# Kernel tuning notes

Measured on AMD Instinct MI355X. Metric: run time of the kernel, lower is better.

The kernel has to match this reference:

```python
import jax, jax.numpy as jnp
import numpy as np

B, T, U = 4, 256, 64
D_ENC = D_PRED = 512
JOINT = 1024
VOCAB = 1024


def setup_inputs() -> dict:
    key = jax.random.key(0)
    ks = jax.random.split(key, 8)
    s = lambda d: 1.0 / np.sqrt(d)
    return {
        "enc": jax.random.normal(ks[0], (B, T, D_ENC), jnp.float32),
        "pred": jax.random.normal(ks[1], (B, U, D_PRED), jnp.float32),
        "W_enc": jax.random.normal(ks[2], (D_ENC, JOINT), jnp.float32) * s(D_ENC),
        "b_enc": jnp.zeros((JOINT,), jnp.float32),
        "W_pred": jax.random.normal(ks[3], (D_PRED, JOINT), jnp.float32) * s(D_PRED),
        "b_pred": jnp.zeros((JOINT,), jnp.float32),
        "W_out": jax.random.normal(ks[4], (JOINT, VOCAB), jnp.float32) * s(JOINT),
        "b_out": jnp.zeros((VOCAB,), jnp.float32),
    }


def reference(enc, pred, W_enc, b_enc, W_pred, b_pred, W_out, b_out):
    # Dense projections to joint_dim
    enc_out = jnp.einsum("btd,dj->btj", enc, W_enc) + b_enc      # [B,T,J]
    pred_out = jnp.einsum("bud,dj->buj", pred, W_pred) + b_pred  # [B,U,J]
    # Broadcast add over (T,U), tanh, then vocab projection
    joint = jnp.tanh(enc_out[:, :, None, :] + pred_out[:, None, :, :])  # [B,T,U,J]
    logits = jnp.einsum("btuj,jv->btuv", joint, W_out) + b_out           # [B,T,U,V]
    return logits
```

## Files before the change

kernel.cpp:

```cpp
#include <hip/hip_runtime.h>
#include <hip/hip_bf16.h>


typedef __bf16 bf16x8 __attribute__((ext_vector_type(8)));
typedef float f32x4 __attribute__((ext_vector_type(4)));
typedef unsigned int u32x4 __attribute__((ext_vector_type(4)));
using bf16_t = __hip_bfloat16;

#define B_ 4
#define T_ 256
#define U_ 64
#define DE 512
#define JD 1024
#define VV 1024

__device__ __forceinline__ void gl2lds16(const void* g, void* l) {
  __builtin_amdgcn_global_load_lds(
      (__attribute__((address_space(1))) void*)(g),
      (__attribute__((address_space(3))) void*)(l), 16, 0, 0);
}

__device__ __forceinline__ float fast_tanh(float x) {
  float xx = fminf(fmaxf(x, -30.f), 30.f);
  float e = __expf(2.f * xx);
  return 1.f - 2.f * __builtin_amdgcn_rcpf(e + 1.f);
}

__device__ __forceinline__ void transpose_body(const float* __restrict__ src,
                                               bf16_t* __restrict__ dst,
                                               int K, int N, int bx, int by, int tid,
                                               float (*tile)[33]) {
  const int nt = bx * 32, kt = by * 32;
  const int tx = tid & 31, ty = tid >> 5;
#pragma unroll
  for (int i = 0; i < 4; ++i)
    tile[ty + i * 8][tx] = src[(size_t)(kt + ty + i * 8) * N + nt + tx];
  __syncthreads();
#pragma unroll
  for (int i = 0; i < 4; ++i)
    dst[(size_t)(nt + ty + i * 8) * K + kt + tx] = __float2bfloat16(tile[tx][ty + i * 8]);
}

__global__ __launch_bounds__(256) void prep_k(
    const float* __restrict__ enc, const float* __restrict__ pred,
    bf16_t* __restrict__ encb, bf16_t* __restrict__ predb,
    const float* __restrict__ W_enc, bf16_t* __restrict__ WtE,
    const float* __restrict__ W_pred, bf16_t* __restrict__ WtP,
    const float* __restrict__ W_out, bf16_t* __restrict__ WtO) {
  __shared__ float tile[32][33];
  const int bid = blockIdx.x, tid = threadIdx.x;
  if (bid < 640) {
    size_t i = ((size_t)bid * 256 + tid) * 4;
    const float* src;
    bf16_t* dst;
    if (i < (size_t)B_ * T_ * DE) { src = enc; dst = encb; }
    else { i -= (size_t)B_ * T_ * DE; src = pred; dst = predb; }
    f32x4 v = *(const f32x4*)(src + i);
    bf16_t o[4];
#pragma unroll
    for (int z = 0; z < 4; ++z) o[z] = __float2bfloat16(v[z]);
    *(unsigned long long*)(dst + i) = *(unsigned long long*)o;
  } else if (bid < 1152) {
    const int lb = bid - 640;
    transpose_body(W_enc, WtE, DE, JD, lb & 31, lb >> 5, tid, tile);
  } else if (bid < 1664) {
    const int lb = bid - 1152;
    transpose_body(W_pred, WtP, DE, JD, lb & 31, lb >> 5, tid, tile);
  } else {
    const int lb = bid - 1664;
    transpose_body(W_out, WtO, JD, VV, lb & 31, lb >> 5, tid, tile);
  }
}

__device__ __forceinline__ void proj_body(const bf16_t* __restrict__ A,
                                          const bf16_t* __restrict__ Bt,
                                          const float* __restrict__ bias,
                                          float* __restrict__ C,
                                          int m0, int n0, int N, int K) {
  __shared__ bf16_t sA[128 * 32];
  __shared__ bf16_t sB[128 * 32];
  const int tid = threadIdx.x;
  const int wave = tid >> 6, lane = tid & 63;
  const int wm = wave >> 1, wn = wave & 1;

  f32x4 acc[4][4] = {};

  for (int k0 = 0; k0 < K; k0 += 32) {
    __syncthreads();
#pragma unroll
    for (int r = 0; r < 2; ++r) {
      const int base = (wave + 4 * r) * 1024;
      const int row  = (base >> 6) + (lane >> 2);
      const int kel  = (lane & 3) * 8;
      gl2lds16(A  + (size_t)(m0 + row) * K + k0 + kel, (char*)sA + base);
      gl2lds16(Bt + (size_t)(n0 + row) * K + k0 + kel, (char*)sB + base);
    }
    __syncthreads();
    bf16x8 af[4], bfr[4];
    const int kq = (lane >> 4) * 8;
#pragma unroll
    for (int i = 0; i < 4; ++i) {
      af[i]  = *(const bf16x8*)(const void*)(sA + (wm * 64 + i * 16 + (lane & 15)) * 32 + kq);
      bfr[i] = *(const bf16x8*)(const void*)(sB + (wn * 64 + i * 16 + (lane & 15)) * 32 + kq);
    }
#pragma unroll
    for (int i = 0; i < 4; ++i)
#pragma unroll
      for (int j = 0; j < 4; ++j)
        acc[i][j] = __builtin_amdgcn_mfma_f32_16x16x32_bf16(af[i], bfr[j], acc[i][j], 0, 0, 0);
  }

  float bv[4];
#pragma unroll
  for (int j = 0; j < 4; ++j) bv[j] = bias[n0 + wn * 64 + j * 16 + (lane & 15)];
#pragma unroll
  for (int i = 0; i < 4; ++i) {
    const int row = m0 + wm * 64 + i * 16 + ((lane >> 4) << 2);
#pragma unroll
    for (int j = 0; j < 4; ++j) {
      const int col = n0 + wn * 64 + j * 16 + (lane & 15);
#pragma unroll
      for (int rr = 0; rr < 4; ++rr)
        C[(size_t)(row + rr) * N + col] = acc[i][j][rr] + bv[j];
    }
  }
}

__global__ __launch_bounds__(256) void proj2_k(
    const bf16_t* __restrict__ encb, const bf16_t* __restrict__ predb,
    const bf16_t* __restrict__ WtE, const bf16_t* __restrict__ WtP,
    const float* __restrict__ b_enc, const float* __restrict__ b_pred,
    float* __restrict__ enc_o, float* __restrict__ pred_o) {
  int bid = blockIdx.x;
  if (bid < 64) {
    proj_body(encb, WtE, b_enc, enc_o, (bid >> 3) * 128, (bid & 7) * 128, JD, DE);
  } else {
    bid -= 64;
    proj_body(predb, WtP, b_pred, pred_o, (bid >> 3) * 128, (bid & 7) * 128, JD, DE);
  }
}


__device__ __forceinline__ void stage_btile(const bf16_t* __restrict__ Bt,
                                            int n0, int k0, char* bb, int wave, int lane) {
  const int rw = lane >> 2;
  const int cl = lane & 3;
#pragma unroll
  for (int g = 0; g < 2; ++g) {
    const int r  = g * 128 + wave * 16 + rw;
    const int cg = cl ^ ((r >> 1) & 3);
    gl2lds16(Bt + (size_t)(n0 + r) * JD + k0 + cg * 8, bb + (g * 128 + wave * 16) * 64);
  }
}

__device__ __forceinline__ void load_ep(const float* __restrict__ enc_o,
                                        const float* __restrict__ pred_o,
                                        int m0, int r, int h, int k0,
                                        f32x4 e[4], f32x4 p[4]) {
  const int m = m0 + r;
  const int enc_row  = m >> 6;
  const int pred_row = ((m >> 14) << 6) | (m & 63);
  const float* pe = enc_o  + (size_t)enc_row  * JD + k0 + h * 16;
  const float* pp = pred_o + (size_t)pred_row * JD + k0 + h * 16;
#pragma unroll
  for (int q = 0; q < 4; ++q) {
    e[q] = *(const f32x4*)(pe + q * 4);
    p[q] = *(const f32x4*)(pp + q * 4);
  }
}

__device__ __forceinline__ void tanh_write_A(const f32x4 e[4], const f32x4 p[4],
                                             char* ab, int r, int h) {
  bf16_t vals[16];
#pragma unroll
  for (int q = 0; q < 4; ++q)
#pragma unroll
    for (int z = 0; z < 4; ++z)
      vals[q * 4 + z] = __float2bfloat16(fast_tanh(e[q][z] + p[q][z]));
  const int key = (r >> 1) & 3;
  *(u32x4*)(void*)(ab + r * 64 + ((2 * h)     ^ key) * 16) = ((const u32x4*)(const void*)vals)[0];
  *(u32x4*)(void*)(ab + r * 64 + ((2 * h + 1) ^ key) * 16) = ((const u32x4*)(const void*)vals)[1];
}

__global__ __launch_bounds__(512, 2) void vocab_fused_k(
    const float* __restrict__ enc_o,
    const float* __restrict__ pred_o,
    const bf16_t* __restrict__ Bt,
    const float* __restrict__ bias,
    float* __restrict__ C) {
  __shared__ char smem[65536];
  const int tid  = threadIdx.x;
  const int wave = tid >> 6, lane = tid & 63;
  const int wm = wave >> 2, wn = wave & 3;

  const int cpx = gridDim.x >> 3;
  const int b   = blockIdx.x;
  const int lb  = (b & 7) * cpx + (b >> 3);
  const int n0  = (lb & 3) * 256;
  const int m0  = (lb >> 2) * 256;

  const int ar = tid >> 1;
  const int ah = tid & 1;

  f32x4 acc[8][4] = {};
  const int NT = JD / 32;

  {
    f32x4 e[4], p[4];
    load_ep(enc_o, pred_o, m0, ar, ah, 0, e, p);
    tanh_write_A(e, p, smem, ar, ah);
    load_ep(enc_o, pred_o, m0, ar, ah, 32, e, p);
    tanh_write_A(e, p, smem + 16384, ar, ah);
  }
  stage_btile(Bt, n0, 0,  smem + 32768, wave, lane);
  stage_btile(Bt, n0, 32, smem + 49152, wave, lane);
  asm volatile("s_waitcnt vmcnt(2) lgkmcnt(0)" ::: "memory");
  __builtin_amdgcn_s_barrier();
  __builtin_amdgcn_sched_barrier(0);

  f32x4 e2[4], p2[4];
  load_ep(enc_o, pred_o, m0, ar, ah, 2 * 32, e2, p2);
  __builtin_amdgcn_sched_barrier(0);

  for (int t = 0; t < NT; ++t) {
    const char* ab = smem + (t & 1) * 16384;
    const char* bb = smem + 32768 + (t & 1) * 16384;
    const int kq = lane >> 4;

    bf16x8 bfr[4];
#pragma unroll
    for (int j = 0; j < 4; ++j) {
      const int rb = wn * 64 + j * 16 + (lane & 15);
      const int cb = kq ^ ((rb >> 1) & 3);
      bfr[j] = *(const bf16x8*)(const void*)(bb + rb * 64 + cb * 16);
    }
#pragma unroll
    for (int mh = 0; mh < 2; ++mh) {
      bf16x8 af[4];
#pragma unroll
      for (int i = 0; i < 4; ++i) {
        const int ra = wm * 128 + mh * 64 + i * 16 + (lane & 15);
        const int ca = kq ^ ((ra >> 1) & 3);
        af[i] = *(const bf16x8*)(const void*)(ab + ra * 64 + ca * 16);
      }
      __builtin_amdgcn_s_setprio(1);
#pragma unroll
      for (int i = 0; i < 4; ++i)
#pragma unroll
        for (int j = 0; j < 4; ++j)
          acc[mh * 4 + i][j] =
              __builtin_amdgcn_mfma_f32_16x16x32_bf16(af[i], bfr[j], acc[mh * 4 + i][j], 0, 0, 0);
      __builtin_amdgcn_s_setprio(0);
    }

    if (t + 1 < NT) {
      __builtin_amdgcn_sched_barrier(0);
      __builtin_amdgcn_s_barrier();
      if (t + 2 < NT) {
        stage_btile(Bt, n0, (t + 2) * 32, (char*)smem + 32768 + (t & 1) * 16384, wave, lane);
        tanh_write_A(e2, p2, (char*)smem + (t & 1) * 16384, ar, ah);
        asm volatile("s_waitcnt vmcnt(2) lgkmcnt(0)" ::: "memory");
      } else {
        asm volatile("s_waitcnt vmcnt(0) lgkmcnt(0)" ::: "memory");
      }
      __builtin_amdgcn_s_barrier();
      __builtin_amdgcn_sched_barrier(0);
      if (t + 3 < NT) {
        load_ep(enc_o, pred_o, m0, ar, ah, (t + 3) * 32, e2, p2);
        __builtin_amdgcn_sched_barrier(0);
      }
    }
  }

  float bv[4];
#pragma unroll
  for (int j = 0; j < 4; ++j) bv[j] = bias[n0 + wn * 64 + j * 16 + (lane & 15)];
#pragma unroll
  for (int i = 0; i < 8; ++i) {
    const int row = m0 + wm * 128 + i * 16 + ((lane >> 4) << 2);
#pragma unroll
    for (int j = 0; j < 4; ++j) {
      const int col = n0 + wn * 64 + j * 16 + (lane & 15);
#pragma unroll
      for (int rr = 0; rr < 4; ++rr)
        C[(size_t)(row + rr) * VV + col] = acc[i][j][rr] + bv[j];
    }
  }
}

extern "C" void kernel_launch(void* const* d_in, const int* in_sizes, int n_in,
                              void* d_out, int out_size, void* d_ws, size_t ws_size,
                              hipStream_t stream) {
  const float* enc    = (const float*)d_in[0];
  const float* pred   = (const float*)d_in[1];
  const float* W_enc  = (const float*)d_in[2];
  const float* b_enc  = (const float*)d_in[3];
  const float* W_pred = (const float*)d_in[4];
  const float* b_pred = (const float*)d_in[5];
  const float* W_out  = (const float*)d_in[6];
  const float* b_out  = (const float*)d_in[7];
  float* out = (float*)d_out;

  char* ws = (char*)d_ws;
  bf16_t* encb   = (bf16_t*)(ws + 0x000000);
  bf16_t* predb  = (bf16_t*)(ws + 0x100000);
  bf16_t* WtE    = (bf16_t*)(ws + 0x140000);
  bf16_t* WtP    = (bf16_t*)(ws + 0x240000);
  bf16_t* WtO    = (bf16_t*)(ws + 0x340000);
  float*  enc_o  = (float*) (ws + 0x540000);
  float*  pred_o = (float*) (ws + 0x940000);

  prep_k<<<2688, 256, 0, stream>>>(enc, pred, encb, predb, W_enc, WtE, W_pred, WtP, W_out, WtO);

  proj2_k<<<80, 256, 0, stream>>>(encb, predb, WtE, WtP, b_enc, b_pred, enc_o, pred_o);

  vocab_fused_k<<<dim3(((B_*T_*U_) / 256) * (VV / 256)), 512, 0, stream>>>(
      enc_o, pred_o, WtO, b_out, out);
}
```

Before: 496.7 us.

## Unfuse tanh into separate materialization kernel and stage A/B via registers

```diff
diff --git a/kernel.cpp b/kernel.cpp
--- a/kernel.cpp
+++ b/kernel.cpp
@@ -140,51 +140,33 @@
   }
 }
 
-
-__device__ __forceinline__ void stage_btile(const bf16_t* __restrict__ Bt,
-                                            int n0, int k0, char* bb, int wave, int lane) {
-  const int rw = lane >> 2;
-  const int cl = lane & 3;
-#pragma unroll
-  for (int g = 0; g < 2; ++g) {
-    const int r  = g * 128 + wave * 16 + rw;
-    const int cg = cl ^ ((r >> 1) & 3);
-    gl2lds16(Bt + (size_t)(n0 + r) * JD + k0 + cg * 8, bb + (g * 128 + wave * 16) * 64);
-  }
-}
-
-__device__ __forceinline__ void load_ep(const float* __restrict__ enc_o,
-                                        const float* __restrict__ pred_o,
-                                        int m0, int r, int h, int k0,
-                                        f32x4 e[4], f32x4 p[4]) {
-  const int m = m0 + r;
+__global__ __launch_bounds__(256) void tanh_mat_k(
+    const float* __restrict__ enc_o,
+    const float* __restrict__ pred_o,
+    bf16_t* __restrict__ joint) {
+  size_t i = ((size_t)blockIdx.x * 256 + threadIdx.x) * 8;
+  const int m = (int)(i >> 10);
+  const int j = (int)(i & 1023);
   const int enc_row  = m >> 6;
   const int pred_row = ((m >> 14) << 6) | (m & 63);
-  const float* pe = enc_o  + (size_t)enc_row  * JD + k0 + h * 16;
-  const float* pp = pred_o + (size_t)pred_row * JD + k0 + h * 16;
-#pragma unroll
-  for (int q = 0; q < 4; ++q) {
-    e[q] = *(const f32x4*)(pe + q * 4);
-    p[q] = *(const f32x4*)(pp + q * 4);
-  }
-}
-
-__device__ __forceinline__ void tanh_write_A(const f32x4 e[4], const f32x4 p[4],
-                                             char* ab, int r, int h) {
-  bf16_t vals[16];
-#pragma unroll
-  for (int q = 0; q < 4; ++q)
+  const f32x4* pe = (const f32x4*)(enc_o  + (size_t)enc_row  * JD + j);
+  const f32x4* pp = (const f32x4*)(pred_o + (size_t)pred_row * JD + j);
+  bf16_t vals[8];
+#pragma unroll
+  for (int q = 0; q < 2; ++q) {
+    f32x4 e = pe[q], p = pp[q];
 #pragma unroll
     for (int z = 0; z < 4; ++z)
-      vals[q * 4 + z] = __float2bfloat16(fast_tanh(e[q][z] + p[q][z]));
-  const int key = (r >> 1) & 3;
-  *(u32x4*)(void*)(ab + r * 64 + ((2 * h)     ^ key) * 16) = ((const u32x4*)(const void*)vals)[0];
-  *(u32x4*)(void*)(ab + r * 64 + ((2 * h + 1) ^ key) * 16) = ((const u32x4*)(const void*)vals)[1];
-}
-
-__global__ __launch_bounds__(512, 2) void vocab_fused_k(
-    const float* __restrict__ enc_o,
-    const float* __restrict__ pred_o,
+      vals[q * 4 + z] = __float2bfloat16(fast_tanh(e[z] + p[z]));
+  }
+  *(u32x4*)(void*)(joint + i) = *(const u32x4*)(const void*)vals;
+}
+
+
+struct RS { u32x4 v[4]; };
+
+__global__ __launch_bounds__(512, 2) void vocab_gemm9_k(
+    const bf16_t* __restrict__ A,
     const bf16_t* __restrict__ Bt,
     const float* __restrict__ bias,
     float* __restrict__ C) {
@@ -199,78 +181,98 @@
   const int n0  = (lb & 3) * 256;
   const int m0  = (lb >> 2) * 256;
 
-  const int ar = tid >> 1;
-  const int ah = tid & 1;
+  const int ra  = tid >> 1;
+  const int c0  = (tid & 1) * 2;
+  const int key = (ra >> 1) & 3;
+  const bf16_t* pa = A  + (size_t)(m0 + ra) * JD;
+  const bf16_t* pb = Bt + (size_t)(n0 + ra) * JD;
+  const int go0 = c0 * 8, go1 = (c0 + 1) * 8;
+  const int lo0 = ((c0 ^ key)) * 16, lo1 = ((c0 + 1) ^ key) * 16;
+
+  char* abuf[2] = { smem, smem + 32768 };
 
   f32x4 acc[8][4] = {};
   const int NT = JD / 32;
 
-  {
-    f32x4 e[4], p[4];
-    load_ep(enc_o, pred_o, m0, ar, ah, 0, e, p);
-    tanh_write_A(e, p, smem, ar, ah);
-    load_ep(enc_o, pred_o, m0, ar, ah, 32, e, p);
-    tanh_write_A(e, p, smem + 16384, ar, ah);
-  }
-  stage_btile(Bt, n0, 0,  smem + 32768, wave, lane);
-  stage_btile(Bt, n0, 32, smem + 49152, wave, lane);
-  asm volatile("s_waitcnt vmcnt(2) lgkmcnt(0)" ::: "memory");
-  __builtin_amdgcn_s_barrier();
-  __builtin_amdgcn_sched_barrier(0);
-
-  f32x4 e2[4], p2[4];
-  load_ep(enc_o, pred_o, m0, ar, ah, 2 * 32, e2, p2);
-  __builtin_amdgcn_sched_barrier(0);
-
-  for (int t = 0; t < NT; ++t) {
-    const char* ab = smem + (t & 1) * 16384;
-    const char* bb = smem + 32768 + (t & 1) * 16384;
-    const int kq = lane >> 4;
-
-    bf16x8 bfr[4];
-#pragma unroll
-    for (int j = 0; j < 4; ++j) {
-      const int rb = wn * 64 + j * 16 + (lane & 15);
-      const int cb = kq ^ ((rb >> 1) & 3);
-      bfr[j] = *(const bf16x8*)(const void*)(bb + rb * 64 + cb * 16);
-    }
-#pragma unroll
-    for (int mh = 0; mh < 2; ++mh) {
-      bf16x8 af[4];
-#pragma unroll
-      for (int i = 0; i < 4; ++i) {
-        const int ra = wm * 128 + mh * 64 + i * 16 + (lane & 15);
-        const int ca = kq ^ ((ra >> 1) & 3);
-        af[i] = *(const bf16x8*)(const void*)(ab + ra * 64 + ca * 16);
-      }
-      __builtin_amdgcn_s_setprio(1);
-#pragma unroll
-      for (int i = 0; i < 4; ++i)
-#pragma unroll
-        for (int j = 0; j < 4; ++j)
-          acc[mh * 4 + i][j] =
-              __builtin_amdgcn_mfma_f32_16x16x32_bf16(af[i], bfr[j], acc[mh * 4 + i][j], 0, 0, 0);
-      __builtin_amdgcn_s_setprio(0);
-    }
-
-    if (t + 1 < NT) {
-      __builtin_amdgcn_sched_barrier(0);
-      __builtin_amdgcn_s_barrier();
-      if (t + 2 < NT) {
-        stage_btile(Bt, n0, (t + 2) * 32, (char*)smem + 32768 + (t & 1) * 16384, wave, lane);
-        tanh_write_A(e2, p2, (char*)smem + (t & 1) * 16384, ar, ah);
-        asm volatile("s_waitcnt vmcnt(2) lgkmcnt(0)" ::: "memory");
-      } else {
-        asm volatile("s_waitcnt vmcnt(0) lgkmcnt(0)" ::: "memory");
-      }
-      __builtin_amdgcn_s_barrier();
-      __builtin_amdgcn_sched_barrier(0);
-      if (t + 3 < NT) {
-        load_ep(enc_o, pred_o, m0, ar, ah, (t + 3) * 32, e2, p2);
-        __builtin_amdgcn_sched_barrier(0);
-      }
-    }
-  }
+#define ISSUE(S, K0)                                           \
+  do {                                                         \
+    (S).v[0] = *(const u32x4*)(const void*)(pa + (K0) + go0);  \
+    (S).v[1] = *(const u32x4*)(const void*)(pa + (K0) + go1);  \
+    (S).v[2] = *(const u32x4*)(const void*)(pb + (K0) + go0);  \
+    (S).v[3] = *(const u32x4*)(const void*)(pb + (K0) + go1);  \
+  } while (0)
+
+#define WRITE(S, AB)                                           \
+  do {                                                         \
+    char* ab_ = (AB);                                          \
+    *(u32x4*)(void*)(ab_ + ra * 64 + lo0)         = (S).v[0];  \
+    *(u32x4*)(void*)(ab_ + ra * 64 + lo1)         = (S).v[1];  \
+    *(u32x4*)(void*)(ab_ + 16384 + ra * 64 + lo0) = (S).v[2];  \
+    *(u32x4*)(void*)(ab_ + 16384 + ra * 64 + lo1) = (S).v[3];  \
+  } while (0)
+
+#define BOUND()                                                \
+  do {                                                         \
+    asm volatile("s_waitcnt lgkmcnt(0)" ::: "memory");         \
+    __builtin_amdgcn_s_barrier();                              \
+    __builtin_amdgcn_sched_barrier(0);                         \
+  } while (0)
+
+#define CONSUME(AB)                                                            \
+  do {                                                                         \
+    const char* ab_ = (AB);                                                    \
+    const char* bb_ = ab_ + 16384;                                             \
+    const int kq = lane >> 4;                                                  \
+    bf16x8 bfr[4];                                                             \
+    _Pragma("unroll")                                                          \
+    for (int j = 0; j < 4; ++j) {                                              \
+      const int rb = wn * 64 + j * 16 + (lane & 15);                           \
+      const int cb = kq ^ ((rb >> 1) & 3);                                     \
+      bfr[j] = *(const bf16x8*)(const void*)(bb_ + rb * 64 + cb * 16);         \
+    }                                                                          \
+    _Pragma("unroll")                                                          \
+    for (int mh = 0; mh < 2; ++mh) {                                           \
+      bf16x8 af[4];                                                            \
+      _Pragma("unroll")                                                        \
+      for (int i = 0; i < 4; ++i) {                                            \
+        const int rr_ = wm * 128 + mh * 64 + i * 16 + (lane & 15);             \
+        const int ca = kq ^ ((rr_ >> 1) & 3);                                  \
+        af[i] = *(const bf16x8*)(const void*)(ab_ + rr_ * 64 + ca * 16);       \
+      }                                                                        \
+      __builtin_amdgcn_s_setprio(1);                                           \
+      _Pragma("unroll")                                                        \
+      for (int i = 0; i < 4; ++i)                                              \
+        _Pragma("unroll")                                                      \
+        for (int j = 0; j < 4; ++j)                                            \
+          acc[mh * 4 + i][j] = __builtin_amdgcn_mfma_f32_16x16x32_bf16(        \
+              af[i], bfr[j], acc[mh * 4 + i][j], 0, 0, 0);                     \
+      __builtin_amdgcn_s_setprio(0);                                           \
+    }                                                                          \
+  } while (0)
+
+  RS rsE, rsO;
+  ISSUE(rsE, 0);
+  ISSUE(rsO, 32);
+  WRITE(rsE, abuf[0]);
+  BOUND();
+
+  for (int t = 0; t < NT; t += 2) {
+    if (t + 2 < NT) ISSUE(rsE, (t + 2) * 32);
+    CONSUME(abuf[0]);
+    WRITE(rsO, abuf[1]);
+    BOUND();
+    if (t + 3 < NT) ISSUE(rsO, (t + 3) * 32);
+    CONSUME(abuf[1]);
+    if (t + 2 < NT) {
+      WRITE(rsE, abuf[0]);
+      BOUND();
+    }
+  }
+
+#undef ISSUE
+#undef WRITE
+#undef BOUND
+#undef CONSUME
 
   float bv[4];
 #pragma unroll
@@ -309,11 +311,11 @@
   bf16_t* WtO    = (bf16_t*)(ws + 0x340000);
   float*  enc_o  = (float*) (ws + 0x540000);
   float*  pred_o = (float*) (ws + 0x940000);
+  bf16_t* joint  = (bf16_t*)(ws + 0xA40000);
 
   prep_k<<<2688, 256, 0, stream>>>(enc, pred, encb, predb, W_enc, WtE, W_pred, WtP, W_out, WtO);
-
   proj2_k<<<80, 256, 0, stream>>>(encb, predb, WtE, WtP, b_enc, b_pred, enc_o, pred_o);
-
-  vocab_fused_k<<<dim3(((B_*T_*U_) / 256) * (VV / 256)), 512, 0, stream>>>(
-      enc_o, pred_o, WtO, b_out, out);
-}
+  tanh_mat_k<<<(B_*T_*U_) * JD / (8 * 256), 256, 0, stream>>>(enc_o, pred_o, joint);
+  vocab_gemm9_k<<<dim3(((B_*T_*U_) / 256) * (VV / 256)), 512, 0, stream>>>(
+      joint, WtO, b_out, out);
+}
```

Result: faster. 462.8 us (-6.8%).
